# Kernel optimization log

Hardware: AMD Instinct MI355X
Metric: run time of the kernel (lower is better)

The kernel has to match this reference:

```python
import jax, jax.numpy as jnp
import numpy as np

# Geometry of the single LocallyConnected2d layer being decomposed
FACTOR = 2      # number of sublayers the out_channels are split into
KH = KW = 3     # kernel size
DH = DW = 1     # stride
OH = OW = 32    # output spatial size
B, C_IN, C_OUT = 128, 32, 64
H = W = OH + KH - 1  # 34 (valid unfold with stride 1)


def setup_inputs() -> dict:
    key = jax.random.key(0)
    kx, kw_, kb = jax.random.split(key, 3)
    x = jax.random.normal(kx, (B, C_IN, H, W), dtype=jnp.float32)
    # per-location weights: (out_ch, in_ch, oh, ow, kh*kw) -- no weight sharing
    weight = jax.random.normal(kw_, (C_OUT, C_IN, OH, OW, KH * KW), dtype=jnp.float32) * 0.05
    bias = jax.random.normal(kb, (C_OUT, OH, OW), dtype=jnp.float32)
    return {"x": x, "weight": weight, "bias": bias}


def _unfold(x):
    # x: (B, C, H, W) -> patches: (B, C, OH, OW, KH*KW)
    # equivalent to torch x.unfold(2,kh,dh).unfold(3,kw,dw).reshape(..., kh*kw)
    cols = [x[:, :, i:i + DH * OH:DH, j:j + DW * OW:DW]
            for i in range(KH) for j in range(KW)]
    return jnp.stack(cols, axis=-1)


def reference(x, weight, bias):
    patches = _unfold(x)  # (B, C, OH, OW, K2)
    new_ch = weight.shape[0] // FACTOR
    outs = []
    for g in range(FACTOR):  # decomposed sublayers, concatenated on channel dim
        w_g = weight[g * new_ch:(g + 1) * new_ch]
        b_g = bias[g * new_ch:(g + 1) * new_ch]
        # out[b,o,i,j] = sum_{c,k} patches[b,c,i,j,k] * w[o,c,i,j,k] + b[o,i,j]
        o_g = jnp.einsum('bcijk,ocijk->boij', patches, w_g) + b_g[None]
        outs.append(o_g)
    return jnp.concatenate(outs, axis=1)  # (B, C_OUT, OH, OW)
```

## Files before the change

### kernel.cpp

```cpp
#include <hip/hip_runtime.h>
#include <cstdint>
#include <cstddef>

#define B_    128
#define C_    32
#define O_    64
#define H_    34
#define NPOS  1024
#define K9    9
#define BC    (B_ * C_)
#define BO    (B_ * O_)
#define NPK   (NPOS * K9)

typedef __bf16 v8bf __attribute__((ext_vector_type(8)));
typedef float  v4f  __attribute__((ext_vector_type(4)));
typedef float  f4a  __attribute__((ext_vector_type(4)));

__device__ __forceinline__ unsigned short f2bf(float f) {
    union { float f; unsigned int u; } v; v.f = f;
    unsigned int u = v.u;
    return (unsigned short)((u + 0x7FFFu + ((u >> 16) & 1u)) >> 16);
}

__global__ __launch_bounds__(256) void repack_x(const float* __restrict__ x,
                                                unsigned short* __restrict__ x2) {
    const int bq = blockIdx.x / 17;
    const int hp = blockIdx.x % 17;
    const int b0 = bq * 2;
    const int h0 = hp * 2;
    __shared__ unsigned short tile[2][H_][66];
    const int t = threadIdx.x;

    for (int e = t; e < 2176; e += 256) {
        const int bb  = e / 1088;
        const int rem = e % 1088;
        const int c   = rem / 34;
        const int wp  = rem % 34;
        const float2 v = *(const float2*)(x +
            ((size_t)((b0 + bb) * C_ + c) * H_ + h0) * H_ + wp * 2);
        const int hh = (wp >= 17) ? 1 : 0;
        const int w  = wp * 2 - hh * 34;
        const int idx = bb * 32 + c;
        tile[hh][w][idx]     = f2bf(v.x);
        tile[hh][w + 1][idx] = f2bf(v.y);
    }
    __syncthreads();

    for (int e = t; e < 2176; e += 256) {
        const int hh  = e / 1088;
        const int rem = e % 1088;
        const int w   = rem >> 5;
        const int i2  = rem & 31;
        ushort2 pk;
        pk.x = tile[hh][w][i2 * 2];
        pk.y = tile[hh][w][i2 * 2 + 1];
        *(ushort2*)(x2 + (size_t)((h0 + hh) * H_ + w) * BC + bq * 64 + i2 * 2) = pk;
    }
}

__global__ __launch_bounds__(512, 1) void lc_fused6(const unsigned short* __restrict__ x2,
                                                    const float* __restrict__ weight,
                                                    const float* __restrict__ bias,
                                                    float* __restrict__ out) {
    __shared__ __align__(16) unsigned short Wl[36 * 2048];

    const int bid = blockIdx.x;
    const int lb  = (bid & 7) * 32 + (bid >> 3);
    const int i   = lb >> 3;
    const int jq  = lb & 7;
    const int j0  = jq * 4;
    const int posbase = i * 32 + j0;
    const int t = threadIdx.x;

    const float* wbase = weight + (size_t)posbase * K9;
#pragma unroll
    for (int r = 0; r < 3; ++r) {
        f4a v[12];
#pragma unroll
        for (int m = 0; m < 12; ++m) {
            const int task = (r * 12 + m) * 512 + t;
            const int pl = task / 9;
            const int d4 = task % 9;
            v[m] = *(const f4a*)(wbase + (size_t)pl * NPK + d4 * 4);
        }
#pragma unroll
        for (int m = 0; m < 12; ++m) {
            const int task = (r * 12 + m) * 512 + t;
            const int pl = task / 9;
            const int d4 = task % 9;
            const int col = (((pl >> 3) ^ (d4 & 7)) << 3) + (pl & 7);
#pragma unroll
            for (int u = 0; u < 4; ++u)
                Wl[(d4 * 4 + u) * 2048 + col] = f2bf(v[m][u]);
        }
    }
    __syncthreads();

    const int wv = t >> 6;
    const int l  = t & 63;
    const int lm = l & 15;
    const int q  = l >> 4;

    v4f acc[4][4];
#pragma unroll
    for (int a = 0; a < 4; ++a)
#pragma unroll
        for (int n = 0; n < 4; ++n) acc[a][n] = (v4f){0.f, 0.f, 0.f, 0.f};

#pragma unroll
    for (int kh = 0; kh < 3; ++kh) {
        v8bf ax[6];
        const int rowbase = (i + kh) * H_ + j0;
#pragma unroll
        for (int w6 = 0; w6 < 6; ++w6) {
            const unsigned short* xrow = x2 + (size_t)(rowbase + w6) * BC;
            ax[w6] = *(const v8bf*)(xrow + (wv * 16 + lm) * C_ + q * 8);
        }
#pragma unroll
        for (int kw = 0; kw < 3; ++kw) {
            const int tap = kh * 3 + kw;
#pragma unroll
            for (int jj = 0; jj < 4; ++jj) {
                const int jk = jj * K9 + tap;
                const int xr = (jk >> 2) & 7;
#pragma unroll
                for (int nt = 0; nt < 4; ++nt) {
                    const int p8 = (nt * 16 + lm) * 4 + q;
                    const v8bf bfr = *(const v8bf*)&Wl[jk * 2048 + ((p8 ^ xr) << 3)];
                    acc[jj][nt] = __builtin_amdgcn_mfma_f32_16x16x32_bf16(
                        ax[kw + jj], bfr, acc[jj][nt], 0, 0, 0);
                }
            }
        }
    }

#pragma unroll
    for (int nt = 0; nt < 4; ++nt) {
        const int o = nt * 16 + lm;
        const f4a bv = *(const f4a*)(bias + (size_t)o * NPOS + posbase);
#pragma unroll
        for (int r2 = 0; r2 < 4; ++r2) {
            const int b = wv * 16 + q * 4 + r2;
            f4a val = {acc[0][nt][r2] + bv[0], acc[1][nt][r2] + bv[1],
                       acc[2][nt][r2] + bv[2], acc[3][nt][r2] + bv[3]};
            *(f4a*)(out + ((size_t)b * O_ + o) * NPOS + posbase) = val;
        }
    }
}

__global__ __launch_bounds__(256) void lc_fallback(const float* __restrict__ x,
                                                   const float* __restrict__ weight,
                                                   const float* __restrict__ bias,
                                                   float* __restrict__ out) {
    const int pos = blockIdx.x;
    const int i = pos >> 5, j = pos & 31;
    const int t  = threadIdx.x;
    const int wv = t >> 6;
    const int l  = t & 63;
    const int lm = l & 15;
    const int q  = l >> 4;

    float bv[4];
#pragma unroll
    for (int nt = 0; nt < 4; ++nt)
        bv[nt] = bias[(size_t)(nt * 16 + lm) * NPOS + pos];

    v4f acc[2][4];
#pragma unroll
    for (int a = 0; a < 2; ++a)
#pragma unroll
        for (int n = 0; n < 4; ++n) acc[a][n] = (v4f){0.f, 0.f, 0.f, 0.f};

    for (int k = 0; k < K9; ++k) {
        const int kh = k / 3, kw = k % 3;
        v8bf af[2], bfr[4];
#pragma unroll
        for (int mt = 0; mt < 2; ++mt) {
            const int b = wv * 32 + mt * 16 + lm;
            union { v8bf v; unsigned short s[8]; } u;
#pragma unroll
            for (int cc = 0; cc < 8; ++cc)
                u.s[cc] = f2bf(x[(((size_t)b * C_ + q * 8 + cc) * H_ + (i + kh)) * H_ + (j + kw)]);
            af[mt] = u.v;
        }
#pragma unroll
        for (int nt = 0; nt < 4; ++nt) {
            union { v8bf v; unsigned short s[8]; } u;
#pragma unroll
            for (int cc = 0; cc < 8; ++cc) {
                const int p = (nt * 16 + lm) * C_ + q * 8 + cc;
                u.s[cc] = f2bf(weight[((size_t)p * NPOS + pos) * K9 + k]);
            }
            bfr[nt] = u.v;
        }
#pragma unroll
        for (int mt = 0; mt < 2; ++mt)
#pragma unroll
            for (int nt = 0; nt < 4; ++nt)
                acc[mt][nt] = __builtin_amdgcn_mfma_f32_16x16x32_bf16(
                    af[mt], bfr[nt], acc[mt][nt], 0, 0, 0);
    }
#pragma unroll
    for (int mt = 0; mt < 2; ++mt)
#pragma unroll
        for (int nt = 0; nt < 4; ++nt) {
            const int o = nt * 16 + lm;
#pragma unroll
            for (int r = 0; r < 4; ++r) {
                const int b = wv * 32 + mt * 16 + q * 4 + r;
                out[(size_t)(b * O_ + o) * NPOS + pos] = acc[mt][nt][r] + bv[nt];
            }
        }
}

extern "C" void kernel_launch(void* const* d_in, const int* in_sizes, int n_in,
                              void* d_out, int out_size, void* d_ws, size_t ws_size,
                              hipStream_t stream) {
    const float* x      = (const float*)d_in[0];
    const float* weight = (const float*)d_in[1];
    const float* bias   = (const float*)d_in[2];
    float* out          = (float*)d_out;

    const size_t X2B = (size_t)H_ * H_ * BC * sizeof(unsigned short);

    if (ws_size >= X2B) {
        unsigned short* x2 = (unsigned short*)d_ws;
        repack_x<<<64 * 17, 256, 0, stream>>>(x, x2);
        lc_fused6<<<256, 512, 0, stream>>>(x2, weight, bias, out);
    } else {
        lc_fallback<<<NPOS, 256, 0, stream>>>(x, weight, bias, out);
    }
}
```

Baseline: 160.3 us.

## Split output channels across blocks and stream weights via double-buffered LDS DMA

The fused kernel now splits the 64 output channels into two halves per block, doubling the grid to 512 blocks. The LDS footprint drops from a full 36x2048 bf16 weight tile to small double buffers, and launch bounds allow several blocks per CU. Weights are streamed with global_load_lds DMA, one group of 4 k-slices per stage, converted to bf16 in LDS, and consumed by MFMA while the next stage is prefetched. This targets the serial weight-load prologue and the one-block-per-CU occupancy, at the cost of two barriers per stage, hand-written waitcnt counts, and reloading the x tile for each channel half.

```diff
diff --git a/kernel.cpp b/kernel.cpp
--- a/kernel.cpp
+++ b/kernel.cpp
@@ -9,7 +9,6 @@
 #define NPOS  1024
 #define K9    9
 #define BC    (B_ * C_)
-#define BO    (B_ * O_)
 #define NPK   (NPOS * K9)
 
 typedef __bf16 v8bf __attribute__((ext_vector_type(8)));
@@ -20,6 +19,12 @@
     union { float f; unsigned int u; } v; v.f = f;
     unsigned int u = v.u;
     return (unsigned short)((u + 0x7FFFu + ((u >> 16) & 1u)) >> 16);
+}
+
+__device__ __forceinline__ void dma16(const void* g, void* l) {
+    __builtin_amdgcn_global_load_lds(
+        (const __attribute__((address_space(1))) unsigned int*)g,
+        (__attribute__((address_space(3))) unsigned int*)l, 16, 0, 0);
 }
 
 __global__ __launch_bounds__(256) void repack_x(const float* __restrict__ x,
@@ -58,85 +63,92 @@
     }
 }
 
-__global__ __launch_bounds__(512, 1) void lc_fused6(const unsigned short* __restrict__ x2,
+__global__ __launch_bounds__(512, 4) void lc_fused8(const unsigned short* __restrict__ x2,
                                                     const float* __restrict__ weight,
                                                     const float* __restrict__ bias,
                                                     float* __restrict__ out) {
-    __shared__ __align__(16) unsigned short Wl[36 * 2048];
+    __shared__ __align__(16) float          Ws[2][1024 * 4];
+    __shared__ __align__(16) unsigned short Im[4][1024];
 
     const int bid = blockIdx.x;
-    const int lb  = (bid & 7) * 32 + (bid >> 3);
-    const int i   = lb >> 3;
-    const int jq  = lb & 7;
+    const int lb  = (bid & 7) * 64 + (bid >> 3);
+    const int i   = lb >> 4;
+    const int jq  = (lb >> 1) & 7;
+    const int oh  = lb & 1;
     const int j0  = jq * 4;
+    const int o0  = oh * 32;
     const int posbase = i * 32 + j0;
-    const int t = threadIdx.x;
-
-    const float* wbase = weight + (size_t)posbase * K9;
-#pragma unroll
-    for (int r = 0; r < 3; ++r) {
-        f4a v[12];
-#pragma unroll
-        for (int m = 0; m < 12; ++m) {
-            const int task = (r * 12 + m) * 512 + t;
-            const int pl = task / 9;
-            const int d4 = task % 9;
-            v[m] = *(const f4a*)(wbase + (size_t)pl * NPK + d4 * 4);
-        }
-#pragma unroll
-        for (int m = 0; m < 12; ++m) {
-            const int task = (r * 12 + m) * 512 + t;
-            const int pl = task / 9;
-            const int d4 = task % 9;
-            const int col = (((pl >> 3) ^ (d4 & 7)) << 3) + (pl & 7);
-#pragma unroll
-            for (int u = 0; u < 4; ++u)
-                Wl[(d4 * 4 + u) * 2048 + col] = f2bf(v[m][u]);
-        }
-    }
-    __syncthreads();
-
+    const int t  = threadIdx.x;
     const int wv = t >> 6;
     const int l  = t & 63;
     const int lm = l & 15;
     const int q  = l >> 4;
 
-    v4f acc[4][4];
+    const float* wbase = weight + (size_t)(o0 * C_) * NPK + (size_t)posbase * K9;
+
+#pragma unroll
+    for (int m = 0; m < 2; ++m)
+        dma16(wbase + (size_t)(m * 512 + t) * NPK,
+              &Ws[0][(m * 512 + (wv * 64)) * 4]);
+
+    v4f acc[4][2];
 #pragma unroll
     for (int a = 0; a < 4; ++a)
 #pragma unroll
-        for (int n = 0; n < 4; ++n) acc[a][n] = (v4f){0.f, 0.f, 0.f, 0.f};
-
-#pragma unroll
-    for (int kh = 0; kh < 3; ++kh) {
-        v8bf ax[6];
-        const int rowbase = (i + kh) * H_ + j0;
-#pragma unroll
-        for (int w6 = 0; w6 < 6; ++w6) {
-            const unsigned short* xrow = x2 + (size_t)(rowbase + w6) * BC;
-            ax[w6] = *(const v8bf*)(xrow + (wv * 16 + lm) * C_ + q * 8);
-        }
-#pragma unroll
-        for (int kw = 0; kw < 3; ++kw) {
-            const int tap = kh * 3 + kw;
-#pragma unroll
-            for (int jj = 0; jj < 4; ++jj) {
-                const int jk = jj * K9 + tap;
-                const int xr = (jk >> 2) & 7;
-#pragma unroll
-                for (int nt = 0; nt < 4; ++nt) {
-                    const int p8 = (nt * 16 + lm) * 4 + q;
-                    const v8bf bfr = *(const v8bf*)&Wl[jk * 2048 + ((p8 ^ xr) << 3)];
-                    acc[jj][nt] = __builtin_amdgcn_mfma_f32_16x16x32_bf16(
-                        ax[kw + jj], bfr, acc[jj][nt], 0, 0, 0);
-                }
+        for (int n = 0; n < 2; ++n) acc[a][n] = (v4f){0.f, 0.f, 0.f, 0.f};
+
+#pragma unroll
+    for (int p = 0; p < 9; ++p) {
+        v8bf ax[4];
+#pragma unroll
+        for (int u = 0; u < 4; ++u) {
+            const int d   = p * 4 + u;
+            const int jj  = d / 9;
+            const int tap = d % 9;
+            const int kh  = tap / 3, kw = tap % 3;
+            const int row = (i + kh) * H_ + j0 + kw + jj;
+            ax[u] = *(const v8bf*)(x2 + (size_t)row * BC + (wv * 16 + lm) * C_ + q * 8);
+        }
+        if (p < 8) {
+#pragma unroll
+            for (int m = 0; m < 2; ++m)
+                dma16(wbase + (size_t)(m * 512 + t) * NPK + (p + 1) * 4,
+                      &Ws[(p + 1) & 1][(m * 512 + (wv * 64)) * 4]);
+            asm volatile("s_waitcnt vmcnt(6)" ::: "memory");
+        } else {
+            asm volatile("s_waitcnt vmcnt(4)" ::: "memory");
+        }
+        __builtin_amdgcn_s_barrier();
+        __builtin_amdgcn_sched_barrier(0);
+
+#pragma unroll
+        for (int m = 0; m < 2; ++m) {
+            const int slot = m * 512 + t;
+            const f4a v = *(const f4a*)&Ws[p & 1][slot * 4];
+#pragma unroll
+            for (int u = 0; u < 4; ++u)
+                Im[u][slot] = f2bf(v[u]);
+        }
+        asm volatile("s_waitcnt lgkmcnt(0)" ::: "memory");
+        __builtin_amdgcn_s_barrier();
+        __builtin_amdgcn_sched_barrier(0);
+
+#pragma unroll
+        for (int u = 0; u < 4; ++u) {
+            const int d  = p * 4 + u;
+            const int jj = d / 9;
+#pragma unroll
+            for (int nt = 0; nt < 2; ++nt) {
+                const v8bf bfr = *(const v8bf*)&Im[u][(nt * 16 + lm) * 32 + q * 8];
+                acc[jj][nt] = __builtin_amdgcn_mfma_f32_16x16x32_bf16(
+                    ax[u], bfr, acc[jj][nt], 0, 0, 0);
             }
         }
     }
 
 #pragma unroll
-    for (int nt = 0; nt < 4; ++nt) {
-        const int o = nt * 16 + lm;
+    for (int nt = 0; nt < 2; ++nt) {
+        const int o = o0 + nt * 16 + lm;
         const f4a bv = *(const f4a*)(bias + (size_t)o * NPOS + posbase);
 #pragma unroll
         for (int r2 = 0; r2 < 4; ++r2) {
@@ -226,7 +238,7 @@
     if (ws_size >= X2B) {
         unsigned short* x2 = (unsigned short*)d_ws;
         repack_x<<<64 * 17, 256, 0, stream>>>(x, x2);
-        lc_fused6<<<256, 512, 0, stream>>>(x2, weight, bias, out);
+        lc_fused8<<<512, 512, 0, stream>>>(x2, weight, bias, out);
     } else {
         lc_fallback<<<NPOS, 256, 0, stream>>>(x, weight, bias, out);
     }
```

Result: slower. 219.7 us (+37.1%).

## Pre-repack weights to bf16 MFMA layout and DMA them into LDS

Applied to the files above, without the earlier changes.

Adds a separate repack_w kernel that converts the fp32 per-location weights to bf16 in a per-block image laid out for direct MFMA B-operand reads. The main kernel then streams that image into LDS with global_load_lds DMA in two halves and starts computing on the first half while the second is still in flight. Each block now covers 16 positions and 16 output channels instead of 4 positions and all 64 channels. This removes the in-kernel conversion and scattered LDS stores, at the cost of an extra kernel launch, a full weight read-and-write pass through workspace, and a larger workspace requirement.

```diff
diff --git a/kernel.cpp b/kernel.cpp
--- a/kernel.cpp
+++ b/kernel.cpp
@@ -9,17 +9,25 @@
 #define NPOS  1024
 #define K9    9
 #define BC    (B_ * C_)
-#define BO    (B_ * O_)
 #define NPK   (NPOS * K9)
+#define W2IMG (144 * 512)
 
 typedef __bf16 v8bf __attribute__((ext_vector_type(8)));
 typedef float  v4f  __attribute__((ext_vector_type(4)));
 typedef float  f4a  __attribute__((ext_vector_type(4)));
+typedef unsigned short u16x8 __attribute__((ext_vector_type(8)));
+typedef unsigned short u16x4 __attribute__((ext_vector_type(4)));
 
 __device__ __forceinline__ unsigned short f2bf(float f) {
     union { float f; unsigned int u; } v; v.f = f;
     unsigned int u = v.u;
     return (unsigned short)((u + 0x7FFFu + ((u >> 16) & 1u)) >> 16);
+}
+
+__device__ __forceinline__ void dma16(const void* g, void* l) {
+    __builtin_amdgcn_global_load_lds(
+        (const __attribute__((address_space(1))) unsigned int*)g,
+        (__attribute__((address_space(3))) unsigned int*)l, 16, 0, 0);
 }
 
 __global__ __launch_bounds__(256) void repack_x(const float* __restrict__ x,
@@ -58,92 +66,114 @@
     }
 }
 
-__global__ __launch_bounds__(512, 1) void lc_fused6(const unsigned short* __restrict__ x2,
-                                                    const float* __restrict__ weight,
+__global__ __launch_bounds__(512) void repack_w(const float* __restrict__ weight,
+                                                unsigned short* __restrict__ w2) {
+    __shared__ __align__(16) unsigned short tile[2][32][292];
+    const int o  = blockIdx.x >> 2;
+    const int iq = blockIdx.x & 3;
+    const int oq = o >> 4, ol = o & 15;
+    const int t  = threadIdx.x;
+
+    for (int ip = 0; ip < 4; ++ip) {
+        const int i0 = iq * 8 + ip * 2;
+        for (int e = t; e < 4608; e += 512) {
+            const int c = e / 144, f = e % 144;
+            const f4a v = *(const f4a*)(weight +
+                ((size_t)(o * 32 + c) * 1024 + i0 * 32) * 9 + 4 * f);
+            const int flat = 4 * f;
+            const int ii = flat / 288, jk = flat % 288;
+            u16x4 pk;
+#pragma unroll
+            for (int u = 0; u < 4; ++u) pk[u] = f2bf(v[u]);
+            *(u16x4*)&tile[ii][c][jk] = pk;
+        }
+        __syncthreads();
+        for (int e = t; e < 576; e += 512) {
+            const int ii = e / 288, rem = e % 288;
+            const int jh = rem / 144, d = rem % 144;
+            const int jk = jh * 144 + d;
+            unsigned short* dst = w2 +
+                ((size_t)((i0 + ii) * 8 + jh * 4 + oq) * 144 + d) * 512 + ol * 32;
+#pragma unroll
+            for (int s = 0; s < 4; ++s) {
+                u16x8 pk;
+#pragma unroll
+                for (int u = 0; u < 8; ++u) pk[u] = tile[ii][s * 8 + u][jk];
+                *(u16x8*)(dst + s * 8) = pk;
+            }
+        }
+        __syncthreads();
+    }
+}
+
+__global__ __launch_bounds__(512, 1) void lc_fused9(const unsigned short* __restrict__ x2,
+                                                    const unsigned short* __restrict__ w2,
                                                     const float* __restrict__ bias,
                                                     float* __restrict__ out) {
-    __shared__ __align__(16) unsigned short Wl[36 * 2048];
+    __shared__ __align__(16) unsigned short Im[W2IMG];
 
     const int bid = blockIdx.x;
     const int lb  = (bid & 7) * 32 + (bid >> 3);
     const int i   = lb >> 3;
-    const int jq  = lb & 7;
-    const int j0  = jq * 4;
+    const int jh  = (lb >> 2) & 1;
+    const int oq  = lb & 3;
+    const int j0  = jh * 16;
     const int posbase = i * 32 + j0;
-    const int t = threadIdx.x;
-
-    const float* wbase = weight + (size_t)posbase * K9;
-#pragma unroll
-    for (int r = 0; r < 3; ++r) {
-        f4a v[12];
-#pragma unroll
-        for (int m = 0; m < 12; ++m) {
-            const int task = (r * 12 + m) * 512 + t;
-            const int pl = task / 9;
-            const int d4 = task % 9;
-            v[m] = *(const f4a*)(wbase + (size_t)pl * NPK + d4 * 4);
-        }
-#pragma unroll
-        for (int m = 0; m < 12; ++m) {
-            const int task = (r * 12 + m) * 512 + t;
-            const int pl = task / 9;
-            const int d4 = task % 9;
-            const int col = (((pl >> 3) ^ (d4 & 7)) << 3) + (pl & 7);
-#pragma unroll
-            for (int u = 0; u < 4; ++u)
-                Wl[(d4 * 4 + u) * 2048 + col] = f2bf(v[m][u]);
-        }
-    }
-    __syncthreads();
-
-    const int wv = t >> 6;
-    const int l  = t & 63;
-    const int lm = l & 15;
-    const int q  = l >> 4;
-
-    v4f acc[4][4];
-#pragma unroll
-    for (int a = 0; a < 4; ++a)
-#pragma unroll
-        for (int n = 0; n < 4; ++n) acc[a][n] = (v4f){0.f, 0.f, 0.f, 0.f};
-
-#pragma unroll
-    for (int kh = 0; kh < 3; ++kh) {
-        v8bf ax[6];
-        const int rowbase = (i + kh) * H_ + j0;
-#pragma unroll
-        for (int w6 = 0; w6 < 6; ++w6) {
-            const unsigned short* xrow = x2 + (size_t)(rowbase + w6) * BC;
-            ax[w6] = *(const v8bf*)(xrow + (wv * 16 + lm) * C_ + q * 8);
-        }
-#pragma unroll
-        for (int kw = 0; kw < 3; ++kw) {
-            const int tap = kh * 3 + kw;
-#pragma unroll
-            for (int jj = 0; jj < 4; ++jj) {
-                const int jk = jj * K9 + tap;
-                const int xr = (jk >> 2) & 7;
-#pragma unroll
-                for (int nt = 0; nt < 4; ++nt) {
-                    const int p8 = (nt * 16 + lm) * 4 + q;
-                    const v8bf bfr = *(const v8bf*)&Wl[jk * 2048 + ((p8 ^ xr) << 3)];
-                    acc[jj][nt] = __builtin_amdgcn_mfma_f32_16x16x32_bf16(
-                        ax[kw + jj], bfr, acc[jj][nt], 0, 0, 0);
+    const int t  = threadIdx.x;
+    const int wv = t >> 6, l = t & 63, lm = l & 15, q = l >> 4;
+
+    const unsigned short* wsrc = w2 + (size_t)lb * W2IMG;
+#pragma unroll
+    for (int r = 0; r < 18; ++r)
+        dma16(wsrc + (size_t)(r * 512 + t) * 8, &Im[(r * 512 + wv * 64) * 8]);
+
+    v4f acc[16];
+#pragma unroll
+    for (int a = 0; a < 16; ++a) acc[a] = (v4f){0.f, 0.f, 0.f, 0.f};
+
+#pragma unroll
+    for (int h = 0; h < 2; ++h) {
+        if (h == 0) asm volatile("s_waitcnt vmcnt(9)" ::: "memory");
+        else        asm volatile("s_waitcnt vmcnt(0)" ::: "memory");
+        __builtin_amdgcn_s_barrier();
+        __builtin_amdgcn_sched_barrier(0);
+
+#pragma unroll
+        for (int kh = 0; kh < 3; ++kh) {
+            v8bf ax[10];
+            const int rowbase = (i + kh) * H_ + j0 + h * 8;
+#pragma unroll
+            for (int w6 = 0; w6 < 10; ++w6)
+                ax[w6] = *(const v8bf*)(x2 + (size_t)(rowbase + w6) * BC +
+                                        (wv * 16 + lm) * C_ + q * 8);
+#pragma unroll
+            for (int kw = 0; kw < 3; ++kw) {
+#pragma unroll
+                for (int jjl = 0; jjl < 8; ++jjl) {
+                    const int jj = h * 8 + jjl;
+                    const int d  = jj * 9 + kh * 3 + kw;
+                    const v8bf bfr = *(const v8bf*)&Im[d * 512 + lm * 32 + q * 8];
+                    acc[jj] = __builtin_amdgcn_mfma_f32_16x16x32_bf16(
+                        ax[jjl + kw], bfr, acc[jj], 0, 0, 0);
                 }
             }
         }
     }
 
-#pragma unroll
-    for (int nt = 0; nt < 4; ++nt) {
-        const int o = nt * 16 + lm;
-        const f4a bv = *(const f4a*)(bias + (size_t)o * NPOS + posbase);
-#pragma unroll
-        for (int r2 = 0; r2 < 4; ++r2) {
-            const int b = wv * 16 + q * 4 + r2;
-            f4a val = {acc[0][nt][r2] + bv[0], acc[1][nt][r2] + bv[1],
-                       acc[2][nt][r2] + bv[2], acc[3][nt][r2] + bv[3]};
-            *(f4a*)(out + ((size_t)b * O_ + o) * NPOS + posbase) = val;
+    const int o = oq * 16 + lm;
+    const float* bp = bias + (size_t)o * NPOS + posbase;
+    f4a bv[4];
+#pragma unroll
+    for (int s = 0; s < 4; ++s) bv[s] = *(const f4a*)(bp + 4 * s);
+#pragma unroll
+    for (int r2 = 0; r2 < 4; ++r2) {
+        const int b = wv * 16 + q * 4 + r2;
+        float* op = out + ((size_t)b * O_ + o) * NPOS + posbase;
+#pragma unroll
+        for (int s = 0; s < 4; ++s) {
+            f4a v = {acc[s * 4 + 0][r2] + bv[s][0], acc[s * 4 + 1][r2] + bv[s][1],
+                     acc[s * 4 + 2][r2] + bv[s][2], acc[s * 4 + 3][r2] + bv[s][3]};
+            *(f4a*)(op + 4 * s) = v;
         }
     }
 }
@@ -222,11 +252,14 @@
     float* out          = (float*)d_out;
 
     const size_t X2B = (size_t)H_ * H_ * BC * sizeof(unsigned short);
-
-    if (ws_size >= X2B) {
+    const size_t W2B = (size_t)256 * W2IMG * sizeof(unsigned short);
+
+    if (ws_size >= X2B + W2B) {
         unsigned short* x2 = (unsigned short*)d_ws;
+        unsigned short* w2 = (unsigned short*)((char*)d_ws + X2B);
         repack_x<<<64 * 17, 256, 0, stream>>>(x, x2);
-        lc_fused6<<<256, 512, 0, stream>>>(x2, weight, bias, out);
+        repack_w<<<256, 512, 0, stream>>>(weight, w2);
+        lc_fused9<<<256, 512, 0, stream>>>(x2, w2, bias, out);
     } else {
         lc_fallback<<<NPOS, 256, 0, stream>>>(x, weight, bias, out);
     }
```

Result: slower. 188.3 us (+17.5%).
